# Optimization experiments

Measured on AMD Instinct MI355X. Metric: run time of the kernel, lower is better.

Reference implementation:

```python
import jax, jax.numpy as jnp
import numpy as np

VOCAB = 8192
ZC = 32
BETA = 0.25
EPS = 1e-12  # torch F.normalize eps


def l2norm(x):
    return x / jnp.maximum(jnp.linalg.norm(x, axis=-1, keepdims=True), EPS)


def setup_inputs() -> dict:
    key = jax.random.key(0)
    k1, k2 = jax.random.split(key)
    z = jax.random.normal(k1, (16, ZC, 32, 32), dtype=jnp.float32)  # [B, C, H, W]
    emb = jax.random.uniform(k2, (VOCAB, ZC), dtype=jnp.float32,
                             minval=-1.0 / VOCAB, maxval=1.0 / VOCAB)
    emb = l2norm(emb)  # codebook_norm init
    return {"z": z, "embedding": emb}


def reference(z, embedding):
    # b c h w -> b h w c
    zc = jnp.einsum('bchw->bhwc', z)
    z_flat = zc.reshape(-1, ZC)                      # [N, C], N = B*H*W
    # codebook_norm: normalize inputs and codebook
    z_flat = l2norm(z_flat)
    zn = z_flat.reshape(zc.shape)                    # normalized z, [B,H,W,C]
    e = l2norm(embedding)                            # [V, C]
    # squared euclidean distances: ||z||^2 + ||e||^2 - 2 z e^T  -> [N, V]
    d = (jnp.sum(z_flat ** 2, axis=1, keepdims=True)
         + jnp.sum(e ** 2, axis=1)
         - 2.0 * jnp.einsum('nd,vd->nv', z_flat, e))
    idx = jnp.argmin(d, axis=1)                      # [N]
    z_q = l2norm(embedding[idx]).reshape(zc.shape)   # gather + normalize
    commit_loss = BETA * jnp.mean((jax.lax.stop_gradient(z_q) - zn) ** 2)
    vq_loss = jnp.mean((z_q - jax.lax.stop_gradient(zn)) ** 2)
    # straight-through estimator
    z_q = zn + jax.lax.stop_gradient(z_q - zn)
    z_q = jnp.einsum('bhwc->bchw', z_q)
    return z_q, vq_loss, commit_loss
```

## Files before the change

### kernel.cpp

```cpp
#include <hip/hip_runtime.h>

typedef _Float16 f16;
typedef _Float16 f16x8 __attribute__((ext_vector_type(8)));
typedef float f32x4 __attribute__((ext_vector_type(4)));

#define ZC 32
#define HW 1024
#define TPB 256
#define VCH 512
#define ZROWS_BLK 256

__device__ __forceinline__ unsigned int fkey(float x) {
    unsigned int b = __float_as_uint(x);
    return (b & 0x80000000u) ? ~b : (b | 0x80000000u);
}

__global__ void kprep(const float* __restrict__ z, const float* __restrict__ emb,
                      float* __restrict__ e, f16* __restrict__ Eh, f16* __restrict__ El,
                      f16x8* __restrict__ ZFh, f16x8* __restrict__ ZFl,
                      float* __restrict__ Zn,
                      unsigned long long* __restrict__ packed,
                      int N, int V, int zblocks) {
    const int blk = blockIdx.x;
    if (blk < zblocks) {
        int t = blk * TPB + threadIdx.x;
        int lane = t & 63, zt = t >> 6;
        int n = zt * 16 + (lane & 15);
        int b = n >> 10, hw = n & 1023;
        int kb = (lane >> 4) * 8;
        float x[8];
        float s = 0.f;
#pragma unroll
        for (int j = 0; j < 8; ++j) {
            x[j] = z[((size_t)(b * ZC + kb + j)) * HW + hw];
            s += x[j] * x[j];
        }
        s += __shfl_xor(s, 16);
        s += __shfl_xor(s, 32);
        float inv = 1.0f / fmaxf(sqrtf(s), 1e-12f);
        f16x8 h, l;
        float4 zn0, zn1;
#pragma unroll
        for (int j = 0; j < 8; ++j) {
            float xn = x[j] * inv;
            f16 hh = (f16)xn;
            h[j] = hh;
            l[j] = (f16)(xn - (float)hh);
            if (j < 4) ((float*)&zn0)[j] = xn; else ((float*)&zn1)[j - 4] = xn;
        }
        ZFh[t] = h;
        ZFl[t] = l;
        float4* zr = (float4*)(Zn + (size_t)n * ZC + kb);
        zr[0] = zn0; zr[1] = zn1;
        int p0 = blk * 64 + threadIdx.x;
        if (threadIdx.x < 64) packed[p0] = 0ull;
    } else {
        int r = (blk - zblocks) * TPB + threadIdx.x;
        if (r >= V) return;
        const float4* src = reinterpret_cast<const float4*>(emb) + (size_t)r * 8;
        float4 v[8];
        float s = 0.f;
#pragma unroll
        for (int j = 0; j < 8; ++j) {
            v[j] = src[j];
            s += v[j].x * v[j].x + v[j].y * v[j].y + v[j].z * v[j].z + v[j].w * v[j].w;
        }
        float inv = 1.0f / fmaxf(sqrtf(s), 1e-12f);
        float4* dst = reinterpret_cast<float4*>(e) + (size_t)r * 8;
        f16* eh = Eh + (size_t)r * ZC;
        f16* el = El + (size_t)r * ZC;
#pragma unroll
        for (int j = 0; j < 8; ++j) {
            float t0 = v[j].x * inv, t1 = v[j].y * inv, t2 = v[j].z * inv, t3 = v[j].w * inv;
            float4 o; o.x = t0; o.y = t1; o.z = t2; o.w = t3;
            dst[j] = o;
            f16 h0 = (f16)t0, h1 = (f16)t1, h2 = (f16)t2, h3 = (f16)t3;
            eh[4 * j + 0] = h0; eh[4 * j + 1] = h1; eh[4 * j + 2] = h2; eh[4 * j + 3] = h3;
            el[4 * j + 0] = (f16)(t0 - (float)h0);
            el[4 * j + 1] = (f16)(t1 - (float)h1);
            el[4 * j + 2] = (f16)(t2 - (float)h2);
            el[4 * j + 3] = (f16)(t3 - (float)h3);
        }
    }
}

__global__ __launch_bounds__(TPB, 2) void kmfma(const f16x8* __restrict__ ZFh,
                                                const f16x8* __restrict__ ZFl,
                                                const uint4* __restrict__ Eh,
                                                const uint4* __restrict__ El,
                                                unsigned long long* __restrict__ packed,
                                                int Vm1) {
    __shared__ uint4 sEh[VCH * 4];
    __shared__ uint4 sEl[VCH * 4];
    const int tid = threadIdx.x;
    const int cb = blockIdx.x & 15;
    const int zb = blockIdx.x >> 4;

    {
        const uint4* gh = Eh + (size_t)cb * (VCH * 4);
        const uint4* gl = El + (size_t)cb * (VCH * 4);
#pragma unroll
        for (int i = 0; i < 8; ++i) {
            int c = tid + i * TPB;
            int r = c >> 2, q = c & 3;
            int w = (r << 2) | (q ^ ((r >> 1) & 3));
            sEh[w] = gh[c];
            sEl[w] = gl[c];
        }
    }

    const int lane = tid & 63;
    const int wv = tid >> 6;
    const int zt0 = zb * 16 + wv * 4;

    f16x8 Bh[4], Bl[4];
#pragma unroll
    for (int i = 0; i < 4; ++i) {
        Bh[i] = ZFh[(size_t)(zt0 + i) * 64 + lane];
        Bl[i] = ZFl[(size_t)(zt0 + i) * 64 + lane];
    }
    __syncthreads();

    const int r15 = lane & 15, qq = lane >> 4;
    const int laneA = (r15 << 2) | (qq ^ ((r15 >> 1) & 3));

    float bv[4] = {-1e38f, -1e38f, -1e38f, -1e38f};
    int bi[4] = {0, 0, 0, 0};
    int g = cb * VCH + qq * 4;

    for (int ct = 0; ct < VCH / 16; ++ct) {
        f16x8 Ah = *(const f16x8*)&sEh[ct * 64 + laneA];
        f16x8 Al = *(const f16x8*)&sEl[ct * 64 + laneA];
#pragma unroll
        for (int i = 0; i < 4; ++i) {
            f32x4 acc = {0.f, 0.f, 0.f, 0.f};
            acc = __builtin_amdgcn_mfma_f32_16x16x32_f16(Ah, Bh[i], acc, 0, 0, 0);
            acc = __builtin_amdgcn_mfma_f32_16x16x32_f16(Ah, Bl[i], acc, 0, 0, 0);
            acc = __builtin_amdgcn_mfma_f32_16x16x32_f16(Al, Bh[i], acc, 0, 0, 0);
#pragma unroll
            for (int r = 0; r < 4; ++r) {
                float v = acc[r];
                bool gt = v > bv[i];
                bi[i] = gt ? (g + r) : bi[i];
                bv[i] = gt ? v : bv[i];
            }
        }
        g += 16;
    }

#pragma unroll
    for (int i = 0; i < 4; ++i) {
        unsigned long long key =
            ((unsigned long long)fkey(bv[i]) << 32) | (unsigned int)(Vm1 - bi[i]);
        unsigned long long o;
        o = __shfl_xor(key, 16); if (o > key) key = o;
        o = __shfl_xor(key, 32); if (o > key) key = o;
        if (lane < 16) atomicMax(&packed[(size_t)(zt0 + i) * 16 + r15], key);
    }
}

__global__ void kfinal(const float* __restrict__ Zn, const float* __restrict__ e,
                       const unsigned long long* __restrict__ packed,
                       float* __restrict__ out, float* __restrict__ partial, int V) {
    __shared__ float red[TPB];
    int n = blockIdx.x * TPB + threadIdx.x;
    int b = n >> 10, hw = n & 1023;
    unsigned long long p = packed[n];
    int idx = (V - 1) - (int)(unsigned int)(p & 0xFFFFFFFFull);

    const float4* er = reinterpret_cast<const float4*>(e) + (size_t)idx * 8;
    const float4* zr = reinterpret_cast<const float4*>(Zn) + (size_t)n * 8;
    float loss = 0.f;
#pragma unroll
    for (int q = 0; q < 8; ++q) {
        float4 ev = er[q];
        float4 zv = zr[q];
        float d0 = ev.x - zv.x, d1 = ev.y - zv.y;
        float d2 = ev.z - zv.z, d3 = ev.w - zv.w;
        loss += d0 * d0 + d1 * d1 + d2 * d2 + d3 * d3;
        out[((size_t)b * ZC + (4 * q + 0)) * HW + hw] = ev.x;
        out[((size_t)b * ZC + (4 * q + 1)) * HW + hw] = ev.y;
        out[((size_t)b * ZC + (4 * q + 2)) * HW + hw] = ev.z;
        out[((size_t)b * ZC + (4 * q + 3)) * HW + hw] = ev.w;
    }

    red[threadIdx.x] = loss;
    __syncthreads();
    for (int st = TPB / 2; st > 0; st >>= 1) {
        if (threadIdx.x < st) red[threadIdx.x] += red[threadIdx.x + st];
        __syncthreads();
    }
    if (threadIdx.x == 0) partial[blockIdx.x] = red[0];
}

__global__ void kloss(const float* __restrict__ partial, float* __restrict__ out,
                      int nblocks, int NC) {
    int lane = threadIdx.x;
    float s = (lane < nblocks) ? partial[lane] : 0.f;
#pragma unroll
    for (int off = 32; off > 0; off >>= 1) s += __shfl_down(s, off);
    if (lane == 0) {
        float mean = s / (float)NC;
        out[NC] = mean;
        out[NC + 1] = 0.25f * mean;
    }
}

extern "C" void kernel_launch(void* const* d_in, const int* in_sizes, int n_in,
                              void* d_out, int out_size, void* d_ws, size_t ws_size,
                              hipStream_t stream) {
    const float* z = (const float*)d_in[0];
    const float* emb = (const float*)d_in[1];
    float* out = (float*)d_out;

    const int N = in_sizes[0] / ZC;
    const int V = in_sizes[1] / ZC;

    char* ws = (char*)d_ws;
    float* e = (float*)ws;
    f16* Eh = (f16*)(ws + (size_t)V * ZC * 4);
    f16* El = (f16*)(ws + (size_t)V * ZC * 6);
    f16x8* ZFh = (f16x8*)(ws + (size_t)V * ZC * 8);
    f16x8* ZFl = (f16x8*)(ws + (size_t)V * ZC * 8 + (size_t)N * ZC * 2);
    float* Zn = (float*)(ws + (size_t)V * ZC * 8 + (size_t)N * ZC * 4);
    unsigned long long* packed =
        (unsigned long long*)(ws + (size_t)V * ZC * 8 + (size_t)N * ZC * 8);
    float* partial = (float*)((char*)packed + (size_t)N * 8);

    const int zblocks = (N * 4 + TPB - 1) / TPB;
    const int eblocks = (V + TPB - 1) / TPB;

    kprep<<<zblocks + eblocks, TPB, 0, stream>>>(z, emb, e, Eh, El, ZFh, ZFl,
                                                 Zn, packed, N, V, zblocks);
    kmfma<<<(V / VCH) * (N / ZROWS_BLK), TPB, 0, stream>>>(
        ZFh, ZFl, (const uint4*)Eh, (const uint4*)El, packed, V - 1);
    kfinal<<<N / TPB, TPB, 0, stream>>>(Zn, e, packed, out, partial, V);
    kloss<<<1, 64, 0, stream>>>(partial, out, N / TPB, N * ZC);
}
```

Measured before the change: 46.03 us.

## Halve codebook chunk, raise occupancy, and defer per-row argmax index resolution

Cuts the codebook chunk per block from 512 to 256 entries, which halves LDS use and lets launch bounds ask for 4 blocks per CU. Block indexing is reordered so z-tiles vary fastest. The inner argmax loop now takes a max over the four accumulator values, records the winning tile, and keeps the raw values. The exact row index is recovered once at the end, which removes per-element index selects from the hot loop. In exchange there are more blocks and twice as many atomicMax operations per row, plus extra registers to hold the saved values.

```diff
diff --git a/kernel.cpp b/kernel.cpp
--- a/kernel.cpp
+++ b/kernel.cpp
@@ -7,7 +7,7 @@
 #define ZC 32
 #define HW 1024
 #define TPB 256
-#define VCH 512
+#define VCH 256
 #define ZROWS_BLK 256
 
 __device__ __forceinline__ unsigned int fkey(float x) {
@@ -84,7 +84,7 @@
     }
 }
 
-__global__ __launch_bounds__(TPB, 2) void kmfma(const f16x8* __restrict__ ZFh,
+__global__ __launch_bounds__(TPB, 4) void kmfma(const f16x8* __restrict__ ZFh,
                                                 const f16x8* __restrict__ ZFl,
                                                 const uint4* __restrict__ Eh,
                                                 const uint4* __restrict__ El,
@@ -93,14 +93,14 @@
     __shared__ uint4 sEh[VCH * 4];
     __shared__ uint4 sEl[VCH * 4];
     const int tid = threadIdx.x;
-    const int cb = blockIdx.x & 15;
-    const int zb = blockIdx.x >> 4;
+    const int zb = blockIdx.x & 63;
+    const int cb = blockIdx.x >> 6;
 
     {
         const uint4* gh = Eh + (size_t)cb * (VCH * 4);
         const uint4* gl = El + (size_t)cb * (VCH * 4);
 #pragma unroll
-        for (int i = 0; i < 8; ++i) {
+        for (int i = 0; i < 4; ++i) {
             int c = tid + i * TPB;
             int r = c >> 2, q = c & 3;
             int w = (r << 2) | (q ^ ((r >> 1) & 3));
@@ -125,8 +125,10 @@
     const int laneA = (r15 << 2) | (qq ^ ((r15 >> 1) & 3));
 
     float bv[4] = {-1e38f, -1e38f, -1e38f, -1e38f};
-    int bi[4] = {0, 0, 0, 0};
-    int g = cb * VCH + qq * 4;
+    int bct[4] = {0, 0, 0, 0};
+    float sv0[4], sv1[4], sv2[4], sv3[4];
+#pragma unroll
+    for (int i = 0; i < 4; ++i) { sv0[i] = sv1[i] = sv2[i] = sv3[i] = 0.f; }
 
     for (int ct = 0; ct < VCH / 16; ++ct) {
         f16x8 Ah = *(const f16x8*)&sEh[ct * 64 + laneA];
@@ -137,21 +139,26 @@
             acc = __builtin_amdgcn_mfma_f32_16x16x32_f16(Ah, Bh[i], acc, 0, 0, 0);
             acc = __builtin_amdgcn_mfma_f32_16x16x32_f16(Ah, Bl[i], acc, 0, 0, 0);
             acc = __builtin_amdgcn_mfma_f32_16x16x32_f16(Al, Bh[i], acc, 0, 0, 0);
-#pragma unroll
-            for (int r = 0; r < 4; ++r) {
-                float v = acc[r];
-                bool gt = v > bv[i];
-                bi[i] = gt ? (g + r) : bi[i];
-                bv[i] = gt ? v : bv[i];
-            }
-        }
-        g += 16;
+            float t4 = fmaxf(fmaxf(fmaxf(acc[0], acc[1]), acc[2]), acc[3]);
+            bool gt = t4 > bv[i];
+            bct[i] = gt ? ct : bct[i];
+            sv0[i] = gt ? acc[0] : sv0[i];
+            sv1[i] = gt ? acc[1] : sv1[i];
+            sv2[i] = gt ? acc[2] : sv2[i];
+            sv3[i] = gt ? acc[3] : sv3[i];
+            bv[i] = gt ? t4 : bv[i];
+        }
     }
 
 #pragma unroll
     for (int i = 0; i < 4; ++i) {
+        int r3 = (sv2[i] == bv[i]) ? 2 : 3;
+        int r2 = (sv1[i] == bv[i]) ? 1 : r3;
+        int rr = (sv0[i] == bv[i]) ? 0 : r2;
+        int idx = cb * VCH + bct[i] * 16 + qq * 4 + rr;
+
         unsigned long long key =
-            ((unsigned long long)fkey(bv[i]) << 32) | (unsigned int)(Vm1 - bi[i]);
+            ((unsigned long long)fkey(bv[i]) << 32) | (unsigned int)(Vm1 - idx);
         unsigned long long o;
         o = __shfl_xor(key, 16); if (o > key) key = o;
         o = __shfl_xor(key, 32); if (o > key) key = o;
```

Result: faster. 43.14 us (-6.3%).
